# Optimization experiments

Measured on AMD Instinct MI355X. Metric: run time of the kernel, lower is better.

Reference implementation:

```python
import jax, jax.numpy as jnp
import numpy as np

D_MODEL = 768
D_STATE = 16
D_CONV = 4
EXPAND = 2
INNER = EXPAND * D_MODEL  # 1536
BATCH = 2
SEQLEN = 2048


def setup_inputs() -> dict:
    key = jax.random.key(0)
    ks = jax.random.split(key, 8)
    s = 0.02
    return {
        "hidden_states": jax.random.normal(ks[0], (BATCH, SEQLEN, D_MODEL), jnp.float32),
        "in_proj_w": jax.random.normal(ks[1], (2 * INNER, D_MODEL), jnp.float32) * (D_MODEL ** -0.5),
        "out_proj_w": jax.random.normal(ks[2], (D_MODEL, INNER), jnp.float32) * (INNER ** -0.5),
        "dt_proj_w": jax.random.normal(ks[3], (INNER, INNER), jnp.float32) * (INNER ** -0.5),
        "dt_proj_b": jnp.zeros((INNER,), jnp.float32),
        "conv_w": jax.random.normal(ks[4], (INNER, D_CONV), jnp.float32) * s,
        "conv_b": jnp.zeros((INNER,), jnp.float32),
        "A_log": jnp.zeros((INNER, D_STATE), jnp.float32),
        "B_param": jax.random.normal(ks[5], (INNER, D_STATE), jnp.float32) * s,
        "C_param": jax.random.normal(ks[6], (INNER, D_STATE), jnp.float32) * s,
        "D_param": jnp.ones((INNER,), jnp.float32),
        "dt_bias": jnp.zeros((INNER,), jnp.float32),
    }


def reference(hidden_states, in_proj_w, out_proj_w, dt_proj_w, dt_proj_b,
              conv_w, conv_b, A_log, B_param, C_param, D_param, dt_bias):
    # in_proj: (B, L, d_model) -> (B, L, 2*inner); split into projected / gate
    xz = jnp.einsum('bld,od->blo', hidden_states, in_proj_w)
    proj, gate = jnp.split(xz, 2, axis=-1)
    x = jnp.transpose(proj, (0, 2, 1))  # (B, inner, L) channel-first

    # depthwise causal conv (left-pad d_conv-1) + bias + SiLU
    conv = jax.lax.conv_general_dilated(
        x, conv_w[:, None, :], window_strides=(1,),
        padding=[(D_CONV - 1, 0)], feature_group_count=INNER,
        dimension_numbers=('NCH', 'OIH', 'NCH'))
    u = jax.nn.silu(conv + conv_b[None, :, None])  # (B, inner, L)

    # dt projection (1x1 linear on channel-first) + softplus(dt + dt_bias)
    delta = jnp.einsum('oc,bcl->bol', dt_proj_w, u) + dt_proj_b[None, :, None]
    dt = jax.nn.softplus(delta + dt_bias[None, :, None])  # (B, inner, L)

    A = -jnp.exp(A_log)  # (inner, d_state)
    # discretize: dA = exp(dt * A), dBu = dt * u * B   -> (B, inner, L, N)
    dA = jnp.exp(dt[..., None] * A[None, :, None, :])
    dBu = (dt * u)[..., None] * B_param[None, :, None, :]

    dA_t = jnp.moveaxis(dA, 2, 0)    # (L, B, inner, N)
    dBu_t = jnp.moveaxis(dBu, 2, 0)  # (L, B, inner, N)

    def step(h, inp):
        a_t, b_t = inp
        h = a_t * h + b_t                      # (B, inner, N)
        y = jnp.einsum('bdn,dn->bd', h, C_param)
        return h, y

    h0 = jnp.zeros(dA_t.shape[1:], dA.dtype)
    _, ys = jax.lax.scan(step, h0, (dA_t, dBu_t))  # ys: (L, B, inner)
    y = jnp.transpose(ys, (1, 2, 0))               # (B, inner, L)

    z = jnp.transpose(gate, (0, 2, 1))             # (B, inner, L)
    y = (y + D_param[None, :, None] * u) * jax.nn.silu(z)

    # out_proj: (B, inner, L) -> (B, L, d_model)
    return jnp.einsum('bdl,od->blo', y, out_proj_w)
```

## Files before the change

kernel.cpp:

```cpp
#include <hip/hip_runtime.h>
#include <cstdint>
#include <cstddef>

#define D_MODEL 768
#define D_STATE 16
#define D_CONV  4
#define INNER   1536
#define BATCH   2
#define SEQLEN  2048
#define M_TOK   (BATCH * SEQLEN)
#define NCH     (BATCH * INNER)
#define NCHUNK  64
#define CL      (SEQLEN / NCHUNK)

typedef unsigned short u16;
typedef __attribute__((ext_vector_type(4))) unsigned short us4;
typedef __attribute__((ext_vector_type(8))) short bf8;
typedef __attribute__((ext_vector_type(4))) float f32x4;

__device__ __forceinline__ u16 f2bf(float f) {
    uint32_t x = __float_as_uint(f);
    return (u16)((x + 0x7fffu + ((x >> 16) & 1u)) >> 16);
}
__device__ __forceinline__ float bf2f(u16 h) {
    return __uint_as_float(((uint32_t)h) << 16);
}

__global__ __launch_bounds__(256) void cvt_hilo4(
    const float* __restrict__ s0, u16* __restrict__ h0, u16* __restrict__ l0, int n0,
    const float* __restrict__ s1, u16* __restrict__ h1, u16* __restrict__ l1, int n1,
    const float* __restrict__ s2, u16* __restrict__ h2, u16* __restrict__ l2, int n2,
    const float* __restrict__ s3, u16* __restrict__ h3, u16* __restrict__ l3, int n3)
{
    int j = blockIdx.x * 256 + threadIdx.x;
    const float* s; u16* hh; u16* ll;
    if (j < n0) { s = s0; hh = h0; ll = l0; }
    else {
        j -= n0;
        if (j < n1) { s = s1; hh = h1; ll = l1; }
        else {
            j -= n1;
            if (j < n2) { s = s2; hh = h2; ll = l2; }
            else {
                j -= n2;
                if (j >= n3) return;
                s = s3; hh = h3; ll = l3;
            }
        }
    }
    const float4 v = ((const float4*)s)[j];
    us4 h, l;
    h.x = f2bf(v.x); l.x = f2bf(v.x - bf2f(h.x));
    h.y = f2bf(v.y); l.y = f2bf(v.y - bf2f(h.y));
    h.z = f2bf(v.z); l.z = f2bf(v.z - bf2f(h.z));
    h.w = f2bf(v.w); l.w = f2bf(v.w - bf2f(h.w));
    ((us4*)hh)[j] = h;
    ((us4*)ll)[j] = l;
}

template <int MODE, int FRM, int FRN>
__global__ __launch_bounds__(256) void gemm_mfma(
    const u16* __restrict__ Ah_g, const u16* __restrict__ Al_g,
    const u16* __restrict__ Bh_g, const u16* __restrict__ Bl_g,
    float* __restrict__ C, const float* __restrict__ bias1,
    const float* __restrict__ bias2, int M, int N, int K)
{
    constexpr int BM = FRM * 32;
    constexpr int BN = FRN * 32;
    constexpr int SBUF = (BM + BN) * 128;
    __shared__ __align__(16) char smem[SBUF];

    const int tid = threadIdx.x;
    const int w = tid >> 6;
    const int lane = tid & 63;

    const int gx = gridDim.x;
    const int nwg = gx * gridDim.y;
    int f = blockIdx.y * gx + blockIdx.x;
    f = (f & 7) * (nwg >> 3) + (f >> 3);
    const int bm = (f / gx) * BM;
    const int bn = (f % gx) * BN;

    const int wm = (w >> 1) * (FRM * 16);
    const int wn = (w & 1) * (FRN * 16);

    const int g8 = lane & 7;
    const int r8 = lane >> 3;
    const int src = g8 ^ r8;
    const int scol = (src & 3) * 8;
    const bool use_lo = (src & 4) != 0;

    const u16* pA[FRM];
    const u16* pB[FRN];
#pragma unroll
    for (int c = 0; c < FRM; ++c) {
        const int row = w * (FRM * 8) + c * 8 + r8;
        pA[c] = (use_lo ? Al_g : Ah_g) + (size_t)(bm + row) * K + scol;
    }
#pragma unroll
    for (int c = 0; c < FRN; ++c) {
        const int row = w * (FRN * 8) + c * 8 + r8;
        pB[c] = (use_lo ? Bl_g : Bh_g) + (size_t)(bn + row) * K + scol;
    }

    f32x4 acc[FRM][FRN] = {};
    const int fr = lane & 15;
    const int gk = lane >> 4;
    const int ghi = gk ^ (fr & 7);

    for (int k0 = 0; k0 < K; k0 += 32) {
        __syncthreads();
#pragma unroll
        for (int c = 0; c < FRM; ++c)
            __builtin_amdgcn_global_load_lds(
                (const __attribute__((address_space(1))) void*)(pA[c] + k0),
                (__attribute__((address_space(3))) void*)(smem + (w * FRM + c) * 1024),
                16, 0, 0);
#pragma unroll
        for (int c = 0; c < FRN; ++c)
            __builtin_amdgcn_global_load_lds(
                (const __attribute__((address_space(1))) void*)(pB[c] + k0),
                (__attribute__((address_space(3))) void*)(smem + BM * 128 + (w * FRN + c) * 1024),
                16, 0, 0);
        asm volatile("s_waitcnt vmcnt(0)" ::: "memory");
        __syncthreads();

        const char* A0 = smem;
        const char* B0 = smem + BM * 128;
        bf8 ah[FRM], al[FRM], bh[FRN], bl[FRN];
#pragma unroll
        for (int i = 0; i < FRM; ++i) {
            const int row = wm + i * 16 + fr;
            ah[i] = *(const bf8*)(A0 + row * 128 + ghi * 16);
            al[i] = *(const bf8*)(A0 + row * 128 + (ghi ^ 4) * 16);
        }
#pragma unroll
        for (int j = 0; j < FRN; ++j) {
            const int row = wn + j * 16 + fr;
            bh[j] = *(const bf8*)(B0 + row * 128 + ghi * 16);
            bl[j] = *(const bf8*)(B0 + row * 128 + (ghi ^ 4) * 16);
        }
#pragma unroll
        for (int i = 0; i < FRM; ++i)
#pragma unroll
            for (int j = 0; j < FRN; ++j) {
                acc[i][j] = __builtin_amdgcn_mfma_f32_16x16x32_bf16(ah[i], bh[j], acc[i][j], 0, 0, 0);
                acc[i][j] = __builtin_amdgcn_mfma_f32_16x16x32_bf16(ah[i], bl[j], acc[i][j], 0, 0, 0);
                acc[i][j] = __builtin_amdgcn_mfma_f32_16x16x32_bf16(al[i], bh[j], acc[i][j], 0, 0, 0);
            }
    }

    const int r0 = (lane >> 4) * 4;
#pragma unroll
    for (int i = 0; i < FRM; ++i) {
        const int row0 = bm + wm + i * 16 + r0;
#pragma unroll
        for (int j = 0; j < FRN; ++j) {
            const int col = bn + wn + j * 16 + fr;
            float add = 0.f;
            if constexpr (MODE == 1) add = bias1[col] + bias2[col];
#pragma unroll
            for (int r = 0; r < 4; ++r) {
                float v = acc[i][j][r];
                if constexpr (MODE == 1) {
                    const float xx = v + add;
                    v = (xx > 20.f) ? xx : log1pf(expf(xx));
                }
                C[(size_t)(row0 + r) * N + col] = v;
            }
        }
    }
}

__global__ __launch_bounds__(256) void conv_silu_kernel(
    const float* __restrict__ xz, const float* __restrict__ cw,
    const float* __restrict__ cb, u16* __restrict__ uh, u16* __restrict__ ul)
{
    const int idx = blockIdx.x * 256 + threadIdx.x;
    const int c4 = (idx % (INNER / 4)) * 4;
    const int m  = idx / (INNER / 4);
    if (m >= M_TOK) return;
    const int b = m >> 11;
    const int l = m & (SEQLEN - 1);

    float wt[4][4];
#pragma unroll
    for (int i = 0; i < 4; ++i) {
        const float4 wv = *(const float4*)&cw[(c4 + i) * 4];
        wt[i][0] = wv.x; wt[i][1] = wv.y; wt[i][2] = wv.z; wt[i][3] = wv.w;
    }
    const float4 bias = *(const float4*)&cb[c4];
    float a[4] = {bias.x, bias.y, bias.z, bias.w};

#pragma unroll
    for (int j = 0; j < 4; ++j) {
        const int ll = l - 3 + j;
        if (ll >= 0) {
            const float4 x = *(const float4*)&xz[(size_t)(b * SEQLEN + ll) * (2 * INNER) + c4];
            a[0] = fmaf(x.x, wt[0][j], a[0]);
            a[1] = fmaf(x.y, wt[1][j], a[1]);
            a[2] = fmaf(x.z, wt[2][j], a[2]);
            a[3] = fmaf(x.w, wt[3][j], a[3]);
        }
    }
    float o[4];
#pragma unroll
    for (int i = 0; i < 4; ++i) o[i] = a[i] / (1.f + __expf(-a[i]));

    us4 h, lo;
    h.x = f2bf(o[0]); lo.x = f2bf(o[0] - bf2f(h.x));
    h.y = f2bf(o[1]); lo.y = f2bf(o[1] - bf2f(h.y));
    h.z = f2bf(o[2]); lo.z = f2bf(o[2] - bf2f(h.z));
    h.w = f2bf(o[3]); lo.w = f2bf(o[3] - bf2f(h.w));
    const size_t vi = ((size_t)m * INNER + c4) / 4;
    ((us4*)uh)[vi] = h;
    ((us4*)ul)[vi] = lo;
}

__global__ __launch_bounds__(256) void scan_pass1(
    const float* __restrict__ dt, const u16* __restrict__ uh,
    const u16* __restrict__ ul, const float* __restrict__ A_log,
    const float* __restrict__ Bp, float* __restrict__ hend,
    float* __restrict__ Sdt)
{
    const int ch = blockIdx.x * 256 + threadIdx.x;
    const int c = blockIdx.y;
    const int b = (ch >= INNER) ? 1 : 0;
    const int d = ch - b * INNER;

    float A2[D_STATE], Bn[D_STATE];
#pragma unroll
    for (int n = 0; n < D_STATE; n += 4) {
        const float4 av = *(const float4*)&A_log[d * D_STATE + n];
        const float4 bv = *(const float4*)&Bp[d * D_STATE + n];
        A2[n+0] = -expf(av.x) * 1.44269504f; Bn[n+0] = bv.x;
        A2[n+1] = -expf(av.y) * 1.44269504f; Bn[n+1] = bv.y;
        A2[n+2] = -expf(av.z) * 1.44269504f; Bn[n+2] = bv.z;
        A2[n+3] = -expf(av.w) * 1.44269504f; Bn[n+3] = bv.w;
    }

    const size_t base = (size_t)(b * SEQLEN + c * CL) * INNER + d;
    const float* dtp = dt + base;
    const u16* uhp = uh + base;
    const u16* ulp = ul + base;

    float h[D_STATE] = {};
    float S = 0.f;

    float dtv = dtp[0];
    float uv = bf2f(uhp[0]) + bf2f(ulp[0]);

    for (int l = 0; l < CL; ++l) {
        float dtn = 0.f, un = 0.f;
        if (l + 1 < CL) {
            dtn = dtp[(size_t)(l + 1) * INNER];
            un = bf2f(uhp[(size_t)(l + 1) * INNER]) + bf2f(ulp[(size_t)(l + 1) * INNER]);
        }
        const float dtu = dtv * uv;
        S += dtv;
#pragma unroll
        for (int n = 0; n < D_STATE; ++n) {
            const float dA = exp2f(dtv * A2[n]);
            h[n] = fmaf(dA, h[n], dtu * Bn[n]);
        }
        dtv = dtn; uv = un;
    }

#pragma unroll
    for (int n = 0; n < D_STATE; ++n)
        hend[((size_t)c * D_STATE + n) * NCH + ch] = h[n];
    Sdt[(size_t)c * NCH + ch] = S;
}

__global__ __launch_bounds__(256) void scan_combine(
    const float* __restrict__ hend, const float* __restrict__ Sdt,
    const float* __restrict__ A_log, float* __restrict__ h0all)
{
    const int idx = blockIdx.x * 256 + threadIdx.x;
    const int n = idx / NCH;
    const int ch = idx - n * NCH;
    const int b = (ch >= INNER) ? 1 : 0;
    const int d = ch - b * INNER;
    const float A2 = -expf(A_log[d * D_STATE + n]) * 1.44269504f;

    float h0 = 0.f;
    for (int c = 0; c < NCHUNK; ++c) {
        const size_t o = ((size_t)c * D_STATE + n) * NCH + ch;
        h0all[o] = h0;
        const float P = exp2f(A2 * Sdt[(size_t)c * NCH + ch]);
        h0 = fmaf(P, h0, hend[o]);
    }
}

__global__ __launch_bounds__(256) void scan_pass2(
    const float* __restrict__ dt, const u16* __restrict__ uh,
    const u16* __restrict__ ul, const float* __restrict__ xz,
    const float* __restrict__ A_log, const float* __restrict__ Bp,
    const float* __restrict__ Cp, const float* __restrict__ Dp,
    const float* __restrict__ h0all, u16* __restrict__ ygh,
    u16* __restrict__ ygl)
{
    const int ch = blockIdx.x * 256 + threadIdx.x;
    const int c = blockIdx.y;
    const int b = (ch >= INNER) ? 1 : 0;
    const int d = ch - b * INNER;

    float A2[D_STATE], Bn[D_STATE], Cn[D_STATE];
#pragma unroll
    for (int n = 0; n < D_STATE; n += 4) {
        const float4 av = *(const float4*)&A_log[d * D_STATE + n];
        const float4 bv = *(const float4*)&Bp[d * D_STATE + n];
        const float4 cv = *(const float4*)&Cp[d * D_STATE + n];
        A2[n+0] = -expf(av.x) * 1.44269504f; Bn[n+0] = bv.x; Cn[n+0] = cv.x;
        A2[n+1] = -expf(av.y) * 1.44269504f; Bn[n+1] = bv.y; Cn[n+1] = cv.y;
        A2[n+2] = -expf(av.z) * 1.44269504f; Bn[n+2] = bv.z; Cn[n+2] = cv.z;
        A2[n+3] = -expf(av.w) * 1.44269504f; Bn[n+3] = bv.w; Cn[n+3] = cv.w;
    }
    const float Dd = Dp[d];

    float h[D_STATE];
#pragma unroll
    for (int n = 0; n < D_STATE; ++n)
        h[n] = h0all[((size_t)c * D_STATE + n) * NCH + ch];

    const size_t base = (size_t)(b * SEQLEN + c * CL) * INNER + d;
    const float* dtp = dt + base;
    const u16* uhp = uh + base;
    const u16* ulp = ul + base;
    const float* zp = xz + (size_t)(b * SEQLEN + c * CL) * (2 * INNER) + INNER + d;
    u16* yhp = ygh + base;
    u16* ylp = ygl + base;

    float dtv = dtp[0];
    float uv = bf2f(uhp[0]) + bf2f(ulp[0]);
    float zv = zp[0];

    for (int l = 0; l < CL; ++l) {
        float dtn = 0.f, un = 0.f, zn = 0.f;
        if (l + 1 < CL) {
            dtn = dtp[(size_t)(l + 1) * INNER];
            un = bf2f(uhp[(size_t)(l + 1) * INNER]) + bf2f(ulp[(size_t)(l + 1) * INNER]);
            zn = zp[(size_t)(l + 1) * (2 * INNER)];
        }
        const float dtu = dtv * uv;
        float y = 0.f;
#pragma unroll
        for (int n = 0; n < D_STATE; ++n) {
            const float dA = exp2f(dtv * A2[n]);
            h[n] = fmaf(dA, h[n], dtu * Bn[n]);
            y = fmaf(h[n], Cn[n], y);
        }
        const float sig = 1.f / (1.f + __expf(-zv));
        const float val = (y + Dd * uv) * (zv * sig);
        const u16 hv = f2bf(val);
        yhp[(size_t)l * INNER] = hv;
        ylp[(size_t)l * INNER] = f2bf(val - bf2f(hv));
        dtv = dtn; uv = un; zv = zn;
    }
}

extern "C" void kernel_launch(void* const* d_in, const int* in_sizes, int n_in,
                              void* d_out, int out_size, void* d_ws, size_t ws_size,
                              hipStream_t stream)
{
    const float* hs      = (const float*)d_in[0];
    const float* in_w    = (const float*)d_in[1];
    const float* out_w   = (const float*)d_in[2];
    const float* dt_w    = (const float*)d_in[3];
    const float* dt_b    = (const float*)d_in[4];
    const float* conv_w  = (const float*)d_in[5];
    const float* conv_b  = (const float*)d_in[6];
    const float* A_log   = (const float*)d_in[7];
    const float* Bp      = (const float*)d_in[8];
    const float* Cp      = (const float*)d_in[9];
    const float* Dp      = (const float*)d_in[10];
    const float* dt_bias = (const float*)d_in[11];
    float* out = (float*)d_out;

    float* xz    = (float*)d_ws;
    float* dtf   = xz + (size_t)M_TOK * 2 * INNER;
    float* hend  = dtf + (size_t)M_TOK * INNER;
    float* Sdt   = hend + (size_t)NCHUNK * D_STATE * NCH;
    float* h0all = Sdt + (size_t)NCHUNK * NCH;
    u16* uh  = (u16*)(h0all + (size_t)NCHUNK * D_STATE * NCH);
    u16* ul  = uh  + (size_t)M_TOK * INNER;
    u16* hsh = ul  + (size_t)M_TOK * INNER;
    u16* hsl = hsh + (size_t)M_TOK * D_MODEL;
    u16* ygh = hsl + (size_t)M_TOK * D_MODEL;
    u16* ygl = ygh + (size_t)M_TOK * INNER;
    u16* iwh = ygl + (size_t)M_TOK * INNER;
    u16* iwl = iwh + (size_t)2 * INNER * D_MODEL;
    u16* dwh = iwl + (size_t)2 * INNER * D_MODEL;
    u16* dwl = dwh + (size_t)INNER * INNER;
    u16* owh = dwl + (size_t)INNER * INNER;
    u16* owl = owh + (size_t)D_MODEL * INNER;

    const dim3 blk(256);

    {
        const int n0 = M_TOK * D_MODEL / 4;
        const int n1 = 2 * INNER * D_MODEL / 4;
        const int n2 = INNER * INNER / 4;
        const int n3 = D_MODEL * INNER / 4;
        const int ntot = n0 + n1 + n2 + n3;
        cvt_hilo4<<<dim3((ntot + 255) / 256), blk, 0, stream>>>(
            hs, hsh, hsl, n0, in_w, iwh, iwl, n1,
            dt_w, dwh, dwl, n2, out_w, owh, owl, n3);
    }

    gemm_mfma<0, 4, 4><<<dim3(2 * INNER / 128, M_TOK / 128), blk, 0, stream>>>(
        hsh, hsl, iwh, iwl, xz, nullptr, nullptr, M_TOK, 2 * INNER, D_MODEL);

    conv_silu_kernel<<<dim3((M_TOK * (INNER / 4)) / 256), blk, 0, stream>>>(
        xz, conv_w, conv_b, uh, ul);

    gemm_mfma<1, 4, 2><<<dim3(INNER / 64, M_TOK / 128), blk, 0, stream>>>(
        uh, ul, dwh, dwl, dtf, dt_b, dt_bias, M_TOK, INNER, INNER);

    scan_pass1<<<dim3(NCH / 256, NCHUNK), blk, 0, stream>>>(
        dtf, uh, ul, A_log, Bp, hend, Sdt);
    scan_combine<<<dim3((D_STATE * NCH) / 256), blk, 0, stream>>>(
        hend, Sdt, A_log, h0all);
    scan_pass2<<<dim3(NCH / 256, NCHUNK), blk, 0, stream>>>(
        dtf, uh, ul, xz, A_log, Bp, Cp, Dp, h0all, ygh, ygl);

    gemm_mfma<0, 2, 2><<<dim3(D_MODEL / 64, M_TOK / 64), blk, 0, stream>>>(
        ygh, ygl, owh, owl, out, nullptr, nullptr, M_TOK, D_MODEL, INNER);
}
```

Baseline: 336.9 us.

## Double-buffer LDS tiles in split-bf16 MFMA GEMM to overlap loads with compute

Doubles the shared-memory buffer so the global-to-LDS loads for the next K tile are issued before the MFMAs on the current tile run. Partial vmcnt waits let the next tile's loads stay in flight while the current one is consumed. Raw s_barrier with sched_barrier fences replaces __syncthreads, and wave priority is raised around the MFMA section. The cost is twice the LDS per block, which may lower occupancy, and tighter reliance on the exact count of outstanding loads.

```diff
diff --git a/kernel.cpp b/kernel.cpp
--- a/kernel.cpp
+++ b/kernel.cpp
@@ -68,7 +68,7 @@
     constexpr int BM = FRM * 32;
     constexpr int BN = FRN * 32;
     constexpr int SBUF = (BM + BN) * 128;
-    __shared__ __align__(16) char smem[SBUF];
+    __shared__ __align__(16) char smem[2 * SBUF];
 
     const int tid = threadIdx.x;
     const int w = tid >> 6;
@@ -108,25 +108,47 @@
     const int gk = lane >> 4;
     const int ghi = gk ^ (fr & 7);
 
-    for (int k0 = 0; k0 < K; k0 += 32) {
-        __syncthreads();
-#pragma unroll
-        for (int c = 0; c < FRM; ++c)
-            __builtin_amdgcn_global_load_lds(
-                (const __attribute__((address_space(1))) void*)(pA[c] + k0),
-                (__attribute__((address_space(3))) void*)(smem + (w * FRM + c) * 1024),
-                16, 0, 0);
-#pragma unroll
-        for (int c = 0; c < FRN; ++c)
-            __builtin_amdgcn_global_load_lds(
-                (const __attribute__((address_space(1))) void*)(pB[c] + k0),
-                (__attribute__((address_space(3))) void*)(smem + BM * 128 + (w * FRN + c) * 1024),
-                16, 0, 0);
-        asm volatile("s_waitcnt vmcnt(0)" ::: "memory");
-        __syncthreads();
-
-        const char* A0 = smem;
-        const char* B0 = smem + BM * 128;
+    const int nt = K >> 5;
+
+#define STAGE_ALL(pp, kt)                                                           \
+    {                                                                               \
+        char* sb = smem + (pp) * SBUF;                                              \
+        _Pragma("unroll")                                                           \
+        for (int c = 0; c < FRM; ++c)                                               \
+            __builtin_amdgcn_global_load_lds(                                       \
+                (const __attribute__((address_space(1))) void*)(pA[c] + (kt)),      \
+                (__attribute__((address_space(3))) void*)(sb + (w * FRM + c) * 1024), \
+                16, 0, 0);                                                          \
+        _Pragma("unroll")                                                           \
+        for (int c = 0; c < FRN; ++c)                                               \
+            __builtin_amdgcn_global_load_lds(                                       \
+                (const __attribute__((address_space(1))) void*)(pB[c] + (kt)),      \
+                (__attribute__((address_space(3))) void*)(sb + BM * 128 + (w * FRN + c) * 1024), \
+                16, 0, 0);                                                          \
+    }
+
+    STAGE_ALL(0, 0)
+
+    int p = 0;
+    for (int t = 0; t < nt; ++t) {
+        if (t + 1 < nt) {
+            STAGE_ALL(p ^ 1, (t + 1) * 32)
+            if constexpr (FRM + FRN == 8) {
+                asm volatile("s_waitcnt vmcnt(8)" ::: "memory");
+            } else if constexpr (FRM + FRN == 6) {
+                asm volatile("s_waitcnt vmcnt(6)" ::: "memory");
+            } else {
+                asm volatile("s_waitcnt vmcnt(4)" ::: "memory");
+            }
+        } else {
+            asm volatile("s_waitcnt vmcnt(0)" ::: "memory");
+        }
+        __builtin_amdgcn_s_barrier();
+        __builtin_amdgcn_sched_barrier(0);
+        __builtin_amdgcn_s_setprio(1);
+
+        const char* A0 = smem + p * SBUF;
+        const char* B0 = A0 + BM * 128;
         bf8 ah[FRM], al[FRM], bh[FRN], bl[FRN];
 #pragma unroll
         for (int i = 0; i < FRM; ++i) {
@@ -148,7 +170,13 @@
                 acc[i][j] = __builtin_amdgcn_mfma_f32_16x16x32_bf16(ah[i], bl[j], acc[i][j], 0, 0, 0);
                 acc[i][j] = __builtin_amdgcn_mfma_f32_16x16x32_bf16(al[i], bh[j], acc[i][j], 0, 0, 0);
             }
-    }
+
+        __builtin_amdgcn_s_setprio(0);
+        __builtin_amdgcn_sched_barrier(0);
+        __builtin_amdgcn_s_barrier();
+        p ^= 1;
+    }
+#undef STAGE_ALL
 
     const int r0 = (lane >> 4) * 4;
 #pragma unroll
```

Result: no change. 333.1 us (-1.1%).
